# Performance work log

Measured on AMD Instinct MI355X. Metric: run time of the kernel, lower is better.

## Reference

```python
import jax, jax.numpy as jnp
import numpy as np


def setup_inputs() -> dict:
    key = jax.random.key(0)
    x = jax.random.normal(key, (64, 256, 56, 56), dtype=jnp.float32)
    return {"x": x}


def reference(x):
    # Per-sample (over all dims except batch) min/max fake-quantization,
    # then dequantize, then hardtanh(0, 6) == ReLU6.
    B = x.shape[0]
    xf = x.reshape(B, -1)
    m = xf.min(axis=1).reshape((B,) + (1,) * (x.ndim - 1))  # per-sample min
    M = xf.max(axis=1).reshape((B,) + (1,) * (x.ndim - 1))  # per-sample max
    rng = M - m
    q = jnp.round(254.0 * (x - m) / rng - 127.0) / 1000.0
    y = (1000.0 * q + 127.0) * rng / 254.0 + m
    return jnp.clip(y, 0.0, 6.0)
```

## Files before the change

### kernel.cpp

```cpp
#include <hip/hip_runtime.h>
#include <hip/hip_bf16.h>
#include <math.h>


#define SAMPLE_V4    200704
#define NSAMPLES     64
#define BPS_R        16
#define V4_PER_BLK_R 12544
#define BPS_E        98
#define V4_PER_BLK_E 2048

typedef __attribute__((ext_vector_type(4))) float fvec4;

__global__ __launch_bounds__(256) void qr_reduce(const float4* __restrict__ x,
                                                 float* __restrict__ pmin,
                                                 float* __restrict__ pmax) {
    const int s = blockIdx.x >> 4;
    const int b = blockIdx.x & (BPS_R - 1);
    const float4* base = x + (size_t)s * SAMPLE_V4 + (size_t)b * V4_PER_BLK_R;

    float mn = INFINITY, mx = -INFINITY;
    for (int i = threadIdx.x; i < V4_PER_BLK_R; i += 256) {
        float4 v = base[i];
        mn = fminf(mn, fminf(fminf(v.x, v.y), fminf(v.z, v.w)));
        mx = fmaxf(mx, fmaxf(fmaxf(v.x, v.y), fmaxf(v.z, v.w)));
    }
    #pragma unroll
    for (int off = 32; off > 0; off >>= 1) {
        mn = fminf(mn, __shfl_down(mn, off, 64));
        mx = fmaxf(mx, __shfl_down(mx, off, 64));
    }
    __shared__ float smn[4], smx[4];
    const int wave = threadIdx.x >> 6;
    if ((threadIdx.x & 63) == 0) { smn[wave] = mn; smx[wave] = mx; }
    __syncthreads();
    if (threadIdx.x == 0) {
        pmin[blockIdx.x] = fminf(fminf(smn[0], smn[1]), fminf(smn[2], smn[3]));
        pmax[blockIdx.x] = fmaxf(fmaxf(smx[0], smx[1]), fmaxf(smx[2], smx[3]));
    }
}

__device__ __forceinline__ float qr_apply1(float x, float m, float sc, float inv) {
    float k = rintf((x - m) * inv - 127.0f);
    float y = fmaf(k + 127.0f, sc, m);
    return fminf(fmaxf(y, 0.0f), 6.0f);
}

__global__ __launch_bounds__(256) void qr_apply(const float4* __restrict__ x,
                                                float4* __restrict__ y,
                                                const float* __restrict__ pmin,
                                                const float* __restrict__ pmax) {
    const int s = blockIdx.x / BPS_E;
    const int b = blockIdx.x % BPS_E;

    __shared__ float sp[3];
    if (threadIdx.x < 64) {
        float mn = (threadIdx.x < BPS_R) ? pmin[s * BPS_R + threadIdx.x] : INFINITY;
        float mx = (threadIdx.x < BPS_R) ? pmax[s * BPS_R + threadIdx.x] : -INFINITY;
        #pragma unroll
        for (int off = 8; off > 0; off >>= 1) {
            mn = fminf(mn, __shfl_down(mn, off, 64));
            mx = fmaxf(mx, __shfl_down(mx, off, 64));
        }
        if (threadIdx.x == 0) {
            const float rng = mx - mn;
            sp[0] = mn;
            sp[1] = rng * (1.0f / 254.0f);
            sp[2] = 254.0f / rng;
        }
    }
    __syncthreads();
    const float m = sp[0], sc = sp[1], inv = sp[2];

    const size_t off = (size_t)s * SAMPLE_V4 + (size_t)b * V4_PER_BLK_E;
    const float4* xb = x + off;
    fvec4* yb = (fvec4*)(y + off);
    for (int i = threadIdx.x; i < V4_PER_BLK_E; i += 256) {
        float4 v = xb[i];
        fvec4 o;
        o.x = qr_apply1(v.x, m, sc, inv);
        o.y = qr_apply1(v.y, m, sc, inv);
        o.z = qr_apply1(v.z, m, sc, inv);
        o.w = qr_apply1(v.w, m, sc, inv);
        __builtin_nontemporal_store(o, &yb[i]);
    }
}

extern "C" void kernel_launch(void* const* d_in, const int* in_sizes, int n_in,
                              void* d_out, int out_size, void* d_ws, size_t ws_size,
                              hipStream_t stream) {
    const float* x = (const float*)d_in[0];
    float* out = (float*)d_out;

    float* pmin = (float*)d_ws;
    float* pmax = pmin + NSAMPLES * BPS_R;

    qr_reduce<<<NSAMPLES * BPS_R, 256, 0, stream>>>((const float4*)x, pmin, pmax);
    qr_apply<<<NSAMPLES * BPS_E, 256, 0, stream>>>((const float4*)x, (float4*)out,
                                                   pmin, pmax);
}
```

Measured before the change: 370.6 us.

## Fuse min/max reduction and quantize-apply into one cooperative kernel with grid sync

```diff
diff --git a/kernel.cpp b/kernel.cpp
--- a/kernel.cpp
+++ b/kernel.cpp
@@ -1,34 +1,42 @@
 #include <hip/hip_runtime.h>
-#include <hip/hip_bf16.h>
+#include <hip/hip_cooperative_groups.h>
 #include <math.h>
+
+namespace cg = cooperative_groups;
 
 
 #define SAMPLE_V4    200704
 #define NSAMPLES     64
-#define BPS_R        16
-#define V4_PER_BLK_R 12544
-#define BPS_E        98
-#define V4_PER_BLK_E 2048
+#define BPS          16
+#define V4_PER_BLK   12544
 
 typedef __attribute__((ext_vector_type(4))) float fvec4;
 
-__global__ __launch_bounds__(256) void qr_reduce(const float4* __restrict__ x,
-                                                 float* __restrict__ pmin,
-                                                 float* __restrict__ pmax) {
+__device__ __forceinline__ float qr_apply1(float x, float m, float sc, float inv) {
+    float k = rintf((x - m) * inv - 127.0f);
+    float y = fmaf(k + 127.0f, sc, m);
+    return fminf(fmaxf(y, 0.0f), 6.0f);
+}
+
+__global__ __launch_bounds__(256) void qr_fused(const float4* __restrict__ x,
+                                                float4* __restrict__ y,
+                                                float* __restrict__ pmin,
+                                                float* __restrict__ pmax) {
     const int s = blockIdx.x >> 4;
-    const int b = blockIdx.x & (BPS_R - 1);
-    const float4* base = x + (size_t)s * SAMPLE_V4 + (size_t)b * V4_PER_BLK_R;
+    const int b = blockIdx.x & (BPS - 1);
+    const size_t off = (size_t)s * SAMPLE_V4 + (size_t)b * V4_PER_BLK;
+    const float4* xb = x + off;
 
     float mn = INFINITY, mx = -INFINITY;
-    for (int i = threadIdx.x; i < V4_PER_BLK_R; i += 256) {
-        float4 v = base[i];
+    for (int i = threadIdx.x; i < V4_PER_BLK; i += 256) {
+        float4 v = xb[i];
         mn = fminf(mn, fminf(fminf(v.x, v.y), fminf(v.z, v.w)));
         mx = fmaxf(mx, fmaxf(fmaxf(v.x, v.y), fmaxf(v.z, v.w)));
     }
     #pragma unroll
-    for (int off = 32; off > 0; off >>= 1) {
-        mn = fminf(mn, __shfl_down(mn, off, 64));
-        mx = fmaxf(mx, __shfl_down(mx, off, 64));
+    for (int o = 32; o > 0; o >>= 1) {
+        mn = fminf(mn, __shfl_down(mn, o, 64));
+        mx = fmaxf(mx, __shfl_down(mx, o, 64));
     }
     __shared__ float smn[4], smx[4];
     const int wave = threadIdx.x >> 6;
@@ -38,33 +46,21 @@
         pmin[blockIdx.x] = fminf(fminf(smn[0], smn[1]), fminf(smn[2], smn[3]));
         pmax[blockIdx.x] = fmaxf(fmaxf(smx[0], smx[1]), fmaxf(smx[2], smx[3]));
     }
-}
 
-__device__ __forceinline__ float qr_apply1(float x, float m, float sc, float inv) {
-    float k = rintf((x - m) * inv - 127.0f);
-    float y = fmaf(k + 127.0f, sc, m);
-    return fminf(fmaxf(y, 0.0f), 6.0f);
-}
-
-__global__ __launch_bounds__(256) void qr_apply(const float4* __restrict__ x,
-                                                float4* __restrict__ y,
-                                                const float* __restrict__ pmin,
-                                                const float* __restrict__ pmax) {
-    const int s = blockIdx.x / BPS_E;
-    const int b = blockIdx.x % BPS_E;
+    cg::this_grid().sync();
 
     __shared__ float sp[3];
     if (threadIdx.x < 64) {
-        float mn = (threadIdx.x < BPS_R) ? pmin[s * BPS_R + threadIdx.x] : INFINITY;
-        float mx = (threadIdx.x < BPS_R) ? pmax[s * BPS_R + threadIdx.x] : -INFINITY;
+        float fmn = (threadIdx.x < BPS) ? pmin[s * BPS + threadIdx.x] : INFINITY;
+        float fmx = (threadIdx.x < BPS) ? pmax[s * BPS + threadIdx.x] : -INFINITY;
         #pragma unroll
-        for (int off = 8; off > 0; off >>= 1) {
-            mn = fminf(mn, __shfl_down(mn, off, 64));
-            mx = fmaxf(mx, __shfl_down(mx, off, 64));
+        for (int o = 8; o > 0; o >>= 1) {
+            fmn = fminf(fmn, __shfl_down(fmn, o, 64));
+            fmx = fmaxf(fmx, __shfl_down(fmx, o, 64));
         }
         if (threadIdx.x == 0) {
-            const float rng = mx - mn;
-            sp[0] = mn;
+            const float rng = fmx - fmn;
+            sp[0] = fmn;
             sp[1] = rng * (1.0f / 254.0f);
             sp[2] = 254.0f / rng;
         }
@@ -72,10 +68,8 @@
     __syncthreads();
     const float m = sp[0], sc = sp[1], inv = sp[2];
 
-    const size_t off = (size_t)s * SAMPLE_V4 + (size_t)b * V4_PER_BLK_E;
-    const float4* xb = x + off;
     fvec4* yb = (fvec4*)(y + off);
-    for (int i = threadIdx.x; i < V4_PER_BLK_E; i += 256) {
+    for (int i = threadIdx.x; i < V4_PER_BLK; i += 256) {
         float4 v = xb[i];
         fvec4 o;
         o.x = qr_apply1(v.x, m, sc, inv);
@@ -89,13 +83,12 @@
 extern "C" void kernel_launch(void* const* d_in, const int* in_sizes, int n_in,
                               void* d_out, int out_size, void* d_ws, size_t ws_size,
                               hipStream_t stream) {
-    const float* x = (const float*)d_in[0];
-    float* out = (float*)d_out;
+    const float4* x = (const float4*)d_in[0];
+    float4* out = (float4*)d_out;
+    float* pmin = (float*)d_ws;
+    float* pmax = pmin + NSAMPLES * BPS;
 
-    float* pmin = (float*)d_ws;
-    float* pmax = pmin + NSAMPLES * BPS_R;
-
-    qr_reduce<<<NSAMPLES * BPS_R, 256, 0, stream>>>((const float4*)x, pmin, pmax);
-    qr_apply<<<NSAMPLES * BPS_E, 256, 0, stream>>>((const float4*)x, (float4*)out,
-                                                   pmin, pmax);
+    void* args[] = {(void*)&x, (void*)&out, (void*)&pmin, (void*)&pmax};
+    hipLaunchCooperativeKernel((void*)qr_fused, dim3(NSAMPLES * BPS), dim3(256),
+                               args, 0, stream);
 }
```

Result: slower. 486.7 us (+31.3%).
